# Optimization experiments

Hardware: AMD Instinct MI355X
Metric: run time of the kernel (lower is better)

The kernel has to match this reference:

```python
import jax, jax.numpy as jnp
import numpy as np

N_ACC, N_MER, E = 200000, 100000, 500000
D_ACC, D_MER, H, OUT, CLF = 64, 32, 128, 64, 64
EPS_BN = 1e-5


def _sage(x_src, x_dst, ei, Wl, bl, Wr, n_dst):
    # PyG SAGEConv(aggr='mean', normalize=True): lin_l(mean_agg) + lin_r(x_dst), then L2-normalize rows
    msg = x_src[ei[0]]                                            # [E, d_in] gather
    s = jax.ops.segment_sum(msg, ei[1], num_segments=n_dst)       # [n_dst, d_in]
    cnt = jax.ops.segment_sum(jnp.ones((ei.shape[1],), x_src.dtype), ei[1], num_segments=n_dst)
    mean = s / jnp.maximum(cnt, 1.0)[:, None]
    out = mean @ Wl.T + bl + x_dst @ Wr.T                         # [n_dst, d_out]
    norm = jnp.linalg.norm(out, axis=-1, keepdims=True)
    return out / jnp.maximum(norm, 1e-12)


def _bn(x, g, b):
    # BatchNorm1d in training mode (batch statistics, biased var)
    mu = x.mean(0)
    var = x.var(0)
    return (x - mu) / jnp.sqrt(var + EPS_BN) * g + b


def setup_inputs() -> dict:
    key = jax.random.key(0)
    ks = jax.random.split(key, 40)

    def rn(k, shape, scale=0.05):
        return jax.random.normal(k, shape, dtype=jnp.float32) * scale

    inp = {
        'x_account': jax.random.normal(ks[0], (N_ACC, D_ACC), dtype=jnp.float32),
        'x_merchant': jax.random.normal(ks[1], (N_MER, D_MER), dtype=jnp.float32),
        'ei_pays': jnp.stack([jax.random.randint(ks[2], (E,), 0, N_ACC),
                              jax.random.randint(ks[3], (E,), 0, N_MER)]).astype(jnp.int32),
        'ei_rev': jnp.stack([jax.random.randint(ks[4], (E,), 0, N_MER),
                             jax.random.randint(ks[5], (E,), 0, N_ACC)]).astype(jnp.int32),
        'ei_transfer': jnp.stack([jax.random.randint(ks[6], (E,), 0, N_ACC),
                                  jax.random.randint(ks[7], (E,), 0, N_ACC)]).astype(jnp.int32),
        # input projections (Linear with bias)
        'projW_acc': rn(ks[8], (H, D_ACC)), 'projb_acc': rn(ks[9], (H,)),
        'projW_mer': rn(ks[10], (H, D_MER)), 'projb_mer': rn(ks[11], (H,)),
        # SAGE layer params stacked over 3 edge types [pays, rev_pays, transfers]
        'Wl0': rn(ks[12], (3, H, H)), 'bl0': rn(ks[13], (3, H)), 'Wr0': rn(ks[14], (3, H, H)),
        'Wl1': rn(ks[15], (3, H, H)), 'bl1': rn(ks[16], (3, H)), 'Wr1': rn(ks[17], (3, H, H)),
        'Wl2': rn(ks[18], (3, OUT, H)), 'bl2': rn(ks[19], (3, OUT)), 'Wr2': rn(ks[20], (3, OUT, H)),
        # BN params per layer, stacked over node types [account, merchant]
        'bng0': jnp.ones((2, H), jnp.float32), 'bnb0': jnp.zeros((2, H), jnp.float32),
        'bng1': jnp.ones((2, H), jnp.float32), 'bnb1': jnp.zeros((2, H), jnp.float32),
        'bng2': jnp.ones((2, OUT), jnp.float32), 'bnb2': jnp.zeros((2, OUT), jnp.float32),
        # fraud classifier MLP: Linear(OUT,CLF) -> ReLU -> Linear(CLF,1)
        'clfW1': rn(ks[21], (CLF, OUT)), 'clfb1': rn(ks[22], (CLF,)),
        'clfW2': rn(ks[23], (1, CLF)), 'clfb2': rn(ks[24], (1,)),
    }
    return inp


def reference(x_account, x_merchant, ei_pays, ei_rev, ei_transfer,
              projW_acc, projb_acc, projW_mer, projb_mer,
              Wl0, bl0, Wr0, Wl1, bl1, Wr1, Wl2, bl2, Wr2,
              bng0, bnb0, bng1, bnb1, bng2, bnb2,
              clfW1, clfb1, clfW2, clfb2):
    # input projections
    xa = x_account @ projW_acc.T + projb_acc      # [N_ACC, H]
    xm = x_merchant @ projW_mer.T + projb_mer     # [N_MER, H]

    layers = [(Wl0, bl0, Wr0, bng0, bnb0), (Wl1, bl1, Wr1, bng1, bnb1), (Wl2, bl2, Wr2, bng2, bnb2)]
    n_layers = len(layers)
    for i, (Wl, bl, Wr, g, b) in enumerate(layers):
        # HeteroConv with aggr='sum': sum per-edge-type SAGE outputs per dst node type
        out_mer = _sage(xa, xm, ei_pays, Wl[0], bl[0], Wr[0], N_MER)
        out_acc = (_sage(xm, xa, ei_rev, Wl[1], bl[1], Wr[1], N_ACC)
                   + _sage(xa, xa, ei_transfer, Wl[2], bl[2], Wr[2], N_ACC))
        xa = _bn(out_acc, g[0], b[0])
        xm = _bn(out_mer, g[1], b[1])
        if i < n_layers - 1:
            xa = jax.nn.relu(xa)
            xm = jax.nn.relu(xm)
            # dropout is identity in eval mode

    # classifier head on target node type 'account'
    h = jax.nn.relu(xa @ clfW1.T + clfb1)
    logits = h @ clfW2.T + clfb2                   # [N_ACC, 1]
    return logits
```

## Files before the change

kernel.cpp:

```cpp
#include <hip/hip_runtime.h>
#include <cstdint>
#include <cstddef>

#define EPS_BN 1e-5f
#define CIS_CAP 640

typedef unsigned short ushort_t;
typedef _Float16 h8 __attribute__((ext_vector_type(8)));
typedef __attribute__((ext_vector_type(4))) float f32x4;

static inline int idiv(int a, int b) { return (a + b - 1) / b; }

__device__ __forceinline__ float h2f(ushort_t b) {
  _Float16 h; __builtin_memcpy(&h, &b, 2); return (float)h;
}
__device__ __forceinline__ ushort_t f2h(float x) {
  _Float16 h = (_Float16)x; ushort_t b; __builtin_memcpy(&b, &h, 2); return b;
}
__device__ __forceinline__ float hlo(unsigned u) { return h2f((ushort_t)(u & 0xffffu)); }
__device__ __forceinline__ float hhi(unsigned u) { return h2f((ushort_t)(u >> 16)); }
__device__ __forceinline__ int imin(int a, int b) { return a < b ? a : b; }

__global__ void cnt_kernel(const int* __restrict__ ei, int* __restrict__ cnt, int E) {
  int e = blockIdx.x * 256 + threadIdx.x;
  if (e < E) atomicAdd(&cnt[ei[E + e]], 1);
}

#define SCAN_TPB 256
#define SCAN_EPT 16
#define SCAN_EPB (SCAN_TPB * SCAN_EPT)

__global__ __launch_bounds__(SCAN_TPB) void bsum_kernel(const int* __restrict__ cnt,
                                                        int* __restrict__ bsum, int n) {
  __shared__ int sm[SCAN_TPB];
  int lo = blockIdx.x * SCAN_EPB + threadIdx.x * SCAN_EPT;
  int s = 0;
#pragma unroll
  for (int i = 0; i < SCAN_EPT; ++i) { int idx = lo + i; if (idx < n) s += cnt[idx]; }
  sm[threadIdx.x] = s;
  __syncthreads();
  for (int off = SCAN_TPB / 2; off; off >>= 1) {
    if (threadIdx.x < off) sm[threadIdx.x] += sm[threadIdx.x + off];
    __syncthreads();
  }
  if (threadIdx.x == 0) bsum[blockIdx.x] = sm[0];
}

__global__ __launch_bounds__(1024) void bscan_kernel(int* __restrict__ bsum, int nb) {
  __shared__ int sm[1024];
  int t = threadIdx.x;
  int v = (t < nb) ? bsum[t] : 0;
  sm[t] = v;
  __syncthreads();
  for (int off = 1; off < 1024; off <<= 1) {
    int u = (t >= off) ? sm[t - off] : 0;
    __syncthreads();
    sm[t] += u;
    __syncthreads();
  }
  if (t < nb) bsum[t] = sm[t] - v;
}

__global__ __launch_bounds__(SCAN_TPB) void scatter_scan_kernel(
    int* cntcur, const int* __restrict__ bsum,
    int* __restrict__ row_ptr, int n, int total) {
  __shared__ int sm[SCAN_TPB];
  int t = threadIdx.x;
  int lo = blockIdx.x * SCAN_EPB + t * SCAN_EPT;
  int loc[SCAN_EPT];
  int s = 0;
#pragma unroll
  for (int i = 0; i < SCAN_EPT; ++i) {
    int idx = lo + i;
    int c = (idx < n) ? cntcur[idx] : 0;
    loc[i] = s; s += c;
  }
  sm[t] = s;
  __syncthreads();
  for (int off = 1; off < SCAN_TPB; off <<= 1) {
    int u = (t >= off) ? sm[t - off] : 0;
    __syncthreads();
    sm[t] += u;
    __syncthreads();
  }
  int base = sm[t] - s + bsum[blockIdx.x];
#pragma unroll
  for (int i = 0; i < SCAN_EPT; ++i) {
    int idx = lo + i;
    if (idx < n) { int v = base + loc[i]; row_ptr[idx] = v; cntcur[idx] = v; }
  }
  if (blockIdx.x == 0 && t == 0) row_ptr[n] = total;
}

__global__ void fill_kernel(const int* __restrict__ ei, int* __restrict__ cursor,
                            int* __restrict__ col_idx, int E) {
  int e = blockIdx.x * 256 + threadIdx.x;
  if (e < E) {
    int d = ei[E + e];
    int p = atomicAdd(&cursor[d], 1);
    col_idx[p] = ei[e];
  }
}

__global__ void wprep_kernel(const float* __restrict__ Wl, const float* __restrict__ Wr,
                             ushort_t* __restrict__ dst, int DOUT) {
  int idx = blockIdx.x * 256 + threadIdx.x;
  int per_mat = DOUT * 128;
  int total = 3 * 2 * per_mat;
  if (idx >= total) return;
  int et = idx / (2 * per_mat);
  int r = idx % (2 * per_mat);
  int mat = r / per_mat;
  int e = r % per_mat;
  int nrow = e / 128, k = e % 128;
  const float* src = mat ? Wr : Wl;
  float w = src[et * per_mat + nrow * 128 + k];
  int kt = k >> 5, kk = k & 31;
  int pos = kt * DOUT * 32 + nrow * 32 + kk;
  int MB = 4 * DOUT * 32;
  dst[(size_t)et * (8 * DOUT * 32) + (size_t)mat * MB + pos] = f2h(w);
}

__global__ void wprep_one_kernel(const float* __restrict__ W, ushort_t* __restrict__ dst,
                                 int DOUT, int K) {
  int idx = blockIdx.x * 256 + threadIdx.x;
  if (idx >= DOUT * K) return;
  int row = idx / K, k = idx % K;
  int kt = k >> 5, kk = k & 31;
  dst[kt * DOUT * 32 + row * 32 + kk] = f2h(W[idx]);
}

template<int K>
__global__ __launch_bounds__(256, 4) void proj_mfma_kernel(
    const float* __restrict__ X, const ushort_t* __restrict__ WP,
    const float* __restrict__ bias, ushort_t* __restrict__ out, int n) {
  constexpr int KT = K / 32;
  __shared__ __align__(16) ushort_t ah[32][64];
  const int tid = threadIdx.x, lane = tid & 63, wv = tid >> 6;
  const int base = blockIdx.x * 32;

  if (K == 64) {
    for (int r = wv; r < 32; r += 4) {
      int row = base + r;
      float v = (row < n) ? X[(size_t)row * 64 + lane] : 0.f;
      char* rp = (char*)&ah[r][0];
      int swz = (r & 7) << 4;
      *(ushort_t*)(rp + ((2 * lane) ^ swz)) = f2h(v);
    }
  } else {
    for (int r = wv; r < 16; r += 4) {
      int rr = 2 * r + (lane >> 5);
      int row = base + rr;
      int el = lane & 31;
      float v = (row < n) ? X[(size_t)row * K + el] : 0.f;
      char* rp = (char*)&ah[rr][0];
      int swz = (rr & 7) << 4;
      *(ushort_t*)(rp + ((2 * el) ^ swz)) = f2h(v);
    }
  }
  __syncthreads();

  const int rt = wv >> 1, half = wv & 1;
  const int colbase = half * 64;
  const int cn = lane & 15, g = lane >> 4;

  f32x4 acc[4];
#pragma unroll
  for (int ct = 0; ct < 4; ++ct) {
    float b = bias[colbase + ct * 16 + cn];
    acc[ct] = (f32x4){b, b, b, b};
  }

  const int arow = rt * 16 + cn;
  const char* rowp = (const char*)&ah[arow][0];
  const int swz = (arow & 7) << 4;

#pragma unroll
  for (int kt = 0; kt < KT; ++kt) {
    h8 a = *(const h8*)(rowp + ((kt * 64 + g * 16) ^ swz));
#pragma unroll
    for (int ct = 0; ct < 4; ++ct) {
      int wb = kt * 128 * 32 + (colbase + ct * 16 + cn) * 32 + 8 * g;
      h8 wh = *(const h8*)(WP + wb);
      acc[ct] = __builtin_amdgcn_mfma_f32_16x16x32_f16(a, wh, acc[ct], 0, 0, 0);
    }
  }

#pragma unroll
  for (int i = 0; i < 4; ++i) {
    int rloc = rt * 16 + g * 4 + i;
    int row = base + rloc;
    if (row < n) {
      ushort_t* op = out + (size_t)row * 128 + colbase + cn;
#pragma unroll
      for (int ct = 0; ct < 4; ++ct) op[ct * 16] = f2h(acc[ct][i]);
    }
  }
}

__device__ __forceinline__ void acc8(float* s, uint4 v) {
  s[0] += hlo(v.x); s[1] += hhi(v.x);
  s[2] += hlo(v.y); s[3] += hhi(v.y);
  s[4] += hlo(v.z); s[5] += hhi(v.z);
  s[6] += hlo(v.w); s[7] += hhi(v.w);
}

__device__ __forceinline__ void grp_gather(const int* rps, const int* cis,
                                           const int* __restrict__ gci,
                                           const ushort_t* __restrict__ src,
                                           int rr, int wq, float* s) {
  int b0 = rps[0];
  int p = rps[rr] - b0, e = rps[rr + 1] - b0;
  for (; p + 2 <= e; p += 2) {
    int n0 = (p < CIS_CAP) ? cis[p] : gci[b0 + p];
    int n1 = (p + 1 < CIS_CAP) ? cis[p + 1] : gci[b0 + p + 1];
    uint4 v0 = ((const uint4*)(src + (size_t)n0 * 128))[wq];
    uint4 v1 = ((const uint4*)(src + (size_t)n1 * 128))[wq];
    acc8(s, v0);
    acc8(s, v1);
  }
  if (p < e) {
    int n0 = (p < CIS_CAP) ? cis[p] : gci[b0 + p];
    uint4 v0 = ((const uint4*)(src + (size_t)n0 * 128))[wq];
    acc8(s, v0);
  }
}

__device__ __forceinline__ uint4 pack_h8v(const float* s, float rc) {
  uint4 o;
  o.x = (unsigned)f2h(s[0] * rc) | ((unsigned)f2h(s[1] * rc) << 16);
  o.y = (unsigned)f2h(s[2] * rc) | ((unsigned)f2h(s[3] * rc) << 16);
  o.z = (unsigned)f2h(s[4] * rc) | ((unsigned)f2h(s[5] * rc) << 16);
  o.w = (unsigned)f2h(s[6] * rc) | ((unsigned)f2h(s[7] * rc) << 16);
  return o;
}

template<int DOUT>
__global__ __launch_bounds__(256, 8) void sage_mfma_kernel(
    const int* __restrict__ row_ptr, const int* __restrict__ col_idx,
    const ushort_t* __restrict__ xsrc, const ushort_t* __restrict__ xd,
    const ushort_t* __restrict__ Wb, const float* __restrict__ bl,
    ushort_t* __restrict__ out, int n) {
  constexpr int NCT = DOUT / 32;
  constexpr int MB = 4 * DOUT * 32;
  __shared__ __align__(16) ushort_t am[32][128];
  __shared__ int rps[33];
  __shared__ int cis[CIS_CAP];
  __shared__ float ssb[32][2];
  const int tid = threadIdx.x, lane = tid & 63, wv = tid >> 6;
  const int grp = tid >> 4, wq = tid & 15;
  const int base = blockIdx.x * 32;

  if (tid < 33) rps[tid] = row_ptr[imin(base + tid, n)];
  __syncthreads();
  {
    int b0 = rps[0];
    int lim = imin(rps[32] - b0, CIS_CAP);
    for (int i = tid; i < lim; i += 256) cis[i] = col_idx[b0 + i];
  }
  __syncthreads();

  for (int rr = grp; rr < 32; rr += 16) {
    int row = base + rr;
    float s[8] = {0.f, 0.f, 0.f, 0.f, 0.f, 0.f, 0.f, 0.f};
    if (row < n) grp_gather(rps, cis, col_idx, xsrc, rr, wq, s);
    int deg = rps[rr + 1] - rps[rr];
    float rc = (deg > 0) ? 1.f / (float)deg : 0.f;
    int bo = (wq * 16) ^ ((rr & 7) << 4);
    *(uint4*)((char*)&am[rr][0] + bo) = pack_h8v(s, rc);
  }
  __syncthreads();

  const int rt = wv >> 1, half = wv & 1;
  const int colbase = half * (DOUT / 2);
  const int cn = lane & 15, g = lane >> 4;

  f32x4 acc[NCT];
#pragma unroll
  for (int ct = 0; ct < NCT; ++ct) {
    float b = bl[colbase + ct * 16 + cn];
    acc[ct] = (f32x4){b, b, b, b};
  }

  const int arow = rt * 16 + cn;
  const char* amrow = (const char*)&am[arow][0];
  const int axor = (arow & 7) << 4;
  const ushort_t* xrow = xd + (size_t)imin(base + arow, n - 1) * 128;

#pragma unroll
  for (int kt = 0; kt < 4; ++kt) {
    int aoff = (kt * 64 + g * 16) ^ axor;
    h8 a_m = *(const h8*)(amrow + aoff);
    h8 a_x = *(const h8*)((const char*)xrow + kt * 64 + g * 16);
    int nbase = kt * DOUT * 32 + (colbase + cn) * 32 + 8 * g;
#pragma unroll
    for (int ct = 0; ct < NCT; ++ct) {
      int no = nbase + ct * 16 * 32;
      h8 wl = *(const h8*)(Wb + 0 * MB + no);
      h8 wr = *(const h8*)(Wb + 1 * MB + no);
      acc[ct] = __builtin_amdgcn_mfma_f32_16x16x32_f16(a_m, wl, acc[ct], 0, 0, 0);
      acc[ct] = __builtin_amdgcn_mfma_f32_16x16x32_f16(a_x, wr, acc[ct], 0, 0, 0);
    }
  }

  float p[4];
#pragma unroll
  for (int i = 0; i < 4; ++i) {
    float s = 0.f;
#pragma unroll
    for (int ct = 0; ct < NCT; ++ct) s += acc[ct][i] * acc[ct][i];
#pragma unroll
    for (int m = 1; m < 16; m <<= 1) s += __shfl_xor(s, m);
    p[i] = s;
  }
  if (cn == 0) {
#pragma unroll
    for (int i = 0; i < 4; ++i) ssb[rt * 16 + g * 4 + i][half] = p[i];
  }
  __syncthreads();

#pragma unroll
  for (int i = 0; i < 4; ++i) {
    int rloc = rt * 16 + g * 4 + i;
    int row = base + rloc;
    float ss = ssb[rloc][0] + ssb[rloc][1];
    float rn = 1.0f / fmaxf(sqrtf(ss), 1e-12f);
    if (row < n) {
      ushort_t* op = out + (size_t)row * DOUT + colbase + cn;
#pragma unroll
      for (int ct = 0; ct < NCT; ++ct) op[ct * 16] = f2h(acc[ct][i] * rn);
    }
  }
}

template<int DOUT>
__global__ __launch_bounds__(256, 7) void sage2_mfma_kernel(
    const int* __restrict__ rp1, const int* __restrict__ ci1, const ushort_t* __restrict__ src1,
    const int* __restrict__ rp2, const int* __restrict__ ci2, const ushort_t* __restrict__ src2,
    const ushort_t* __restrict__ Wb1, const ushort_t* __restrict__ Wb2,
    const float* __restrict__ bl1, const float* __restrict__ bl2,
    ushort_t* __restrict__ out, int n) {
  constexpr int NCT = DOUT / 32;
  constexpr int MB = 4 * DOUT * 32;
  __shared__ __align__(16) ushort_t a1[32][128];
  __shared__ __align__(16) ushort_t a2[32][128];
  __shared__ int rps1[33], rps2[33];
  __shared__ int cis1[CIS_CAP], cis2[CIS_CAP];
  __shared__ float ssb1[32][2], ssb2[32][2];
  const int tid = threadIdx.x, lane = tid & 63, wv = tid >> 6;
  const int grp = tid >> 4, wq = tid & 15;
  const int base = blockIdx.x * 32;

  if (tid < 33) rps1[tid] = rp1[imin(base + tid, n)];
  else if (tid < 66) rps2[tid - 33] = rp2[imin(base + (tid - 33), n)];
  __syncthreads();
  {
    int b1 = rps1[0];
    int lim1 = imin(rps1[32] - b1, CIS_CAP);
    for (int i = tid; i < lim1; i += 256) cis1[i] = ci1[b1 + i];
    int b2 = rps2[0];
    int lim2 = imin(rps2[32] - b2, CIS_CAP);
    for (int i = tid; i < lim2; i += 256) cis2[i] = ci2[b2 + i];
  }
  __syncthreads();

  for (int rr = grp; rr < 32; rr += 16) {
    int row = base + rr;
    float s1[8] = {0.f, 0.f, 0.f, 0.f, 0.f, 0.f, 0.f, 0.f};
    float s2[8] = {0.f, 0.f, 0.f, 0.f, 0.f, 0.f, 0.f, 0.f};
    if (row < n) {
      grp_gather(rps1, cis1, ci1, src1, rr, wq, s1);
      grp_gather(rps2, cis2, ci2, src2, rr, wq, s2);
    }
    int d1 = rps1[rr + 1] - rps1[rr];
    int d2 = rps2[rr + 1] - rps2[rr];
    float rc1 = (d1 > 0) ? 1.f / (float)d1 : 0.f;
    float rc2 = (d2 > 0) ? 1.f / (float)d2 : 0.f;
    int bo = (wq * 16) ^ ((rr & 7) << 4);
    *(uint4*)((char*)&a1[rr][0] + bo) = pack_h8v(s1, rc1);
    *(uint4*)((char*)&a2[rr][0] + bo) = pack_h8v(s2, rc2);
  }
  __syncthreads();

  const int rt = wv >> 1, half = wv & 1;
  const int colbase = half * (DOUT / 2);
  const int cn = lane & 15, g = lane >> 4;

  f32x4 acc1[NCT], acc2[NCT];
#pragma unroll
  for (int ct = 0; ct < NCT; ++ct) {
    float b1v = bl1[colbase + ct * 16 + cn];
    float b2v = bl2[colbase + ct * 16 + cn];
    acc1[ct] = (f32x4){b1v, b1v, b1v, b1v};
    acc2[ct] = (f32x4){b2v, b2v, b2v, b2v};
  }

  const int arow = rt * 16 + cn;
  const char* r1 = (const char*)&a1[arow][0];
  const char* r2 = (const char*)&a2[arow][0];
  const int axor = (arow & 7) << 4;
  const ushort_t* xrow = src2 + (size_t)imin(base + arow, n - 1) * 128;

#pragma unroll
  for (int kt = 0; kt < 4; ++kt) {
    int aoff = (kt * 64 + g * 16) ^ axor;
    h8 f1 = *(const h8*)(r1 + aoff);
    h8 f2 = *(const h8*)(r2 + aoff);
    h8 fx = *(const h8*)((const char*)xrow + kt * 64 + g * 16);
    int nbase = kt * DOUT * 32 + (colbase + cn) * 32 + 8 * g;
#pragma unroll
    for (int ct = 0; ct < NCT; ++ct) {
      int no = nbase + ct * 16 * 32;
      h8 wl1 = *(const h8*)(Wb1 + 0 * MB + no);
      h8 wr1 = *(const h8*)(Wb1 + 1 * MB + no);
      h8 wl2 = *(const h8*)(Wb2 + 0 * MB + no);
      h8 wr2 = *(const h8*)(Wb2 + 1 * MB + no);
      acc1[ct] = __builtin_amdgcn_mfma_f32_16x16x32_f16(f1, wl1, acc1[ct], 0, 0, 0);
      acc1[ct] = __builtin_amdgcn_mfma_f32_16x16x32_f16(fx, wr1, acc1[ct], 0, 0, 0);
      acc2[ct] = __builtin_amdgcn_mfma_f32_16x16x32_f16(f2, wl2, acc2[ct], 0, 0, 0);
      acc2[ct] = __builtin_amdgcn_mfma_f32_16x16x32_f16(fx, wr2, acc2[ct], 0, 0, 0);
    }
  }

#pragma unroll
  for (int i = 0; i < 4; ++i) {
    float s1 = 0.f, s2 = 0.f;
#pragma unroll
    for (int ct = 0; ct < NCT; ++ct) {
      s1 += acc1[ct][i] * acc1[ct][i];
      s2 += acc2[ct][i] * acc2[ct][i];
    }
#pragma unroll
    for (int m = 1; m < 16; m <<= 1) {
      s1 += __shfl_xor(s1, m);
      s2 += __shfl_xor(s2, m);
    }
    if (cn == 0) {
      ssb1[rt * 16 + g * 4 + i][half] = s1;
      ssb2[rt * 16 + g * 4 + i][half] = s2;
    }
  }
  __syncthreads();

#pragma unroll
  for (int i = 0; i < 4; ++i) {
    int rloc = rt * 16 + g * 4 + i;
    int row = base + rloc;
    float rn1 = 1.0f / fmaxf(sqrtf(ssb1[rloc][0] + ssb1[rloc][1]), 1e-12f);
    float rn2 = 1.0f / fmaxf(sqrtf(ssb2[rloc][0] + ssb2[rloc][1]), 1e-12f);
    if (row < n) {
      ushort_t* op = out + (size_t)row * DOUT + colbase + cn;
#pragma unroll
      for (int ct = 0; ct < NCT; ++ct)
        op[ct * 16] = f2h(acc1[ct][i] * rn1 + acc2[ct][i] * rn2);
    }
  }
}

template<int C>
__global__ __launch_bounds__(256) void bn_stats_kernel(const ushort_t* __restrict__ x,
    float* __restrict__ stats, int n) {
  constexpr int TPR = C / 8;
  constexpr int RPB = 256 / TPR;
  __shared__ float smw[4][TPR][16];
  const int tid = threadIdx.x, lane = tid & 63, wv = tid >> 6;
  const int cg = tid % TPR;
  const int r0 = tid / TPR;

  float s[8] = {0.f, 0.f, 0.f, 0.f, 0.f, 0.f, 0.f, 0.f};
  float q[8] = {0.f, 0.f, 0.f, 0.f, 0.f, 0.f, 0.f, 0.f};
  for (int r = blockIdx.x * RPB + r0; r < n; r += gridDim.x * RPB) {
    uint4 v = ((const uint4*)(x + (size_t)r * C))[cg];
    unsigned w[4] = {v.x, v.y, v.z, v.w};
#pragma unroll
    for (int j = 0; j < 4; ++j) {
      float a = hlo(w[j]), b = hhi(w[j]);
      s[2 * j] += a; q[2 * j] += a * a;
      s[2 * j + 1] += b; q[2 * j + 1] += b * b;
    }
  }
#pragma unroll
  for (int j = 0; j < 8; ++j) {
    for (int m = TPR; m < 64; m <<= 1) {
      s[j] += __shfl_xor(s[j], m);
      q[j] += __shfl_xor(q[j], m);
    }
  }
  if (lane < TPR) {
#pragma unroll
    for (int j = 0; j < 8; ++j) {
      smw[wv][lane][j] = s[j];
      smw[wv][lane][8 + j] = q[j];
    }
  }
  __syncthreads();
  if (tid < C) {
    int g2 = tid >> 3, j = tid & 7;
    float ts = smw[0][g2][j] + smw[1][g2][j] + smw[2][g2][j] + smw[3][g2][j];
    float tq = smw[0][g2][8 + j] + smw[1][g2][8 + j] + smw[2][g2][8 + j] + smw[3][g2][8 + j];
    atomicAdd(&stats[tid], ts);
    atomicAdd(&stats[C + tid], tq);
  }
}

template<int C, bool RELU>
__global__ __launch_bounds__(256) void bn_apply_kernel(ushort_t* __restrict__ x,
    const float* __restrict__ stats, const float* __restrict__ g,
    const float* __restrict__ b, int n) {
  size_t i = (size_t)blockIdx.x * 256 + threadIdx.x;
  size_t total = (size_t)n * C / 8;
  if (i >= total) return;
  int c0 = (int)((i * 8) & (C - 1));
  float rn = 1.f / (float)n;
  uint4 v = ((const uint4*)x)[i];
  unsigned w[4] = {v.x, v.y, v.z, v.w};
  unsigned o[4];
#pragma unroll
  for (int j = 0; j < 4; ++j) {
    int cA = c0 + 2 * j, cB = cA + 1;
    float muA = stats[cA] * rn, muB = stats[cB] * rn;
    float vaA = stats[C + cA] * rn - muA * muA;
    float vaB = stats[C + cB] * rn - muB * muB;
    float xA = (hlo(w[j]) - muA) * rsqrtf(vaA + EPS_BN) * g[cA] + b[cA];
    float xB = (hhi(w[j]) - muB) * rsqrtf(vaB + EPS_BN) * g[cB] + b[cB];
    if (RELU) { xA = fmaxf(xA, 0.f); xB = fmaxf(xB, 0.f); }
    o[j] = (unsigned)f2h(xA) | ((unsigned)f2h(xB) << 16);
  }
  ((uint4*)x)[i] = make_uint4(o[0], o[1], o[2], o[3]);
}

__global__ __launch_bounds__(256, 4) void clf_mfma_kernel(
    const ushort_t* __restrict__ X, const ushort_t* __restrict__ WPc,
    const float* __restrict__ b1, const float* __restrict__ W2,
    const float* __restrict__ b2, float* __restrict__ out, int n) {
  __shared__ __align__(16) ushort_t axl[32][64];
  __shared__ float ssb[32][2];
  const int tid = threadIdx.x, lane = tid & 63, wv = tid >> 6;
  const int base = blockIdx.x * 32;

  for (int r = wv; r < 16; r += 4) {
    int rr = 2 * r + (lane >> 5);
    int row = base + rr;
    int el = lane & 31;
    unsigned v = (row < n) ? ((const unsigned*)(X + (size_t)row * 64))[el] : 0u;
    int swz = (rr & 7) << 4;
    *(unsigned*)((char*)&axl[rr][0] + ((4 * el) ^ swz)) = v;
  }
  __syncthreads();

  const int rt = wv >> 1, half = wv & 1;
  const int colbase = half * 32;
  const int cn = lane & 15, g = lane >> 4;

  f32x4 acc[2];
#pragma unroll
  for (int ct = 0; ct < 2; ++ct) {
    float b = b1[colbase + ct * 16 + cn];
    acc[ct] = (f32x4){b, b, b, b};
  }

  const int arow = rt * 16 + cn;
  const char* rowp = (const char*)&axl[arow][0];
  const int swz = (arow & 7) << 4;

#pragma unroll
  for (int kt = 0; kt < 2; ++kt) {
    h8 a = *(const h8*)(rowp + ((kt * 64 + g * 16) ^ swz));
#pragma unroll
    for (int ct = 0; ct < 2; ++ct) {
      int wb = kt * 64 * 32 + (colbase + ct * 16 + cn) * 32 + 8 * g;
      h8 wh = *(const h8*)(WPc + wb);
      acc[ct] = __builtin_amdgcn_mfma_f32_16x16x32_f16(a, wh, acc[ct], 0, 0, 0);
    }
  }

  float w2v0 = W2[colbase + cn], w2v1 = W2[colbase + 16 + cn];
#pragma unroll
  for (int i = 0; i < 4; ++i) {
    float p = fmaxf(acc[0][i], 0.f) * w2v0 + fmaxf(acc[1][i], 0.f) * w2v1;
#pragma unroll
    for (int m = 1; m < 16; m <<= 1) p += __shfl_xor(p, m);
    if (cn == 0) ssb[rt * 16 + g * 4 + i][half] = p;
  }
  __syncthreads();

  if (tid < 32) {
    int row = base + tid;
    if (row < n) out[row] = ssb[tid][0] + ssb[tid][1] + b2[0];
  }
}

template<int DO, bool RELU>
static void run_layer(const ushort_t* WB, const float* bl,
                      const float* g, const float* b,
                      const ushort_t* xa, const ushort_t* xm,
                      ushort_t* oa, ushort_t* om, float* STATS,
                      const int* rp_p, const int* ci_p,
                      const int* rp_r, const int* ci_r,
                      const int* rp_t, const int* ci_t,
                      int NA, int NM, hipStream_t stream) {
  const size_t ETS = (size_t)8 * DO * 32;
  float* stA = STATS;
  float* stM = STATS + 2 * DO;
  hipMemsetAsync(STATS, 0, 4 * DO * sizeof(float), stream);
  sage_mfma_kernel<DO><<<idiv(NM, 32), 256, 0, stream>>>(
      rp_p, ci_p, xa, xm, WB + 0 * ETS, bl, om, NM);
  sage2_mfma_kernel<DO><<<idiv(NA, 32), 256, 0, stream>>>(
      rp_r, ci_r, xm, rp_t, ci_t, xa,
      WB + 1 * ETS, WB + 2 * ETS, bl + DO, bl + 2 * DO, oa, NA);
  bn_stats_kernel<DO><<<256, 256, 0, stream>>>(oa, stA, NA);
  bn_stats_kernel<DO><<<256, 256, 0, stream>>>(om, stM, NM);
  bn_apply_kernel<DO, RELU><<<idiv(NA * DO / 8, 256), 256, 0, stream>>>(oa, stA, g, b, NA);
  bn_apply_kernel<DO, RELU><<<idiv(NM * DO / 8, 256), 256, 0, stream>>>(om, stM, g + DO, b + DO, NM);
}

static size_t ws_need(int NA, int NM, int E) {
  size_t acts = ((size_t)2 * NA * 128 + (size_t)2 * NM * 128) * 2;
  size_t wbuf = ((size_t)2 * 98304 + 49152 + 8192 + 4096 + 4096) * 2;
  size_t stats = 1024 * 4;
  size_t ints = ((size_t)(NM + 1) + NM + E
               + 2 * ((size_t)(NA + 1) + NA + E) + 1024) * 4;
  return acts + wbuf + stats + ints + 256;
}

extern "C" void kernel_launch(void* const* d_in, const int* in_sizes, int n_in,
                              void* d_out, int out_size, void* d_ws, size_t ws_size,
                              hipStream_t stream) {
  const int NA = in_sizes[0] / 64;
  const int NM = in_sizes[1] / 32;
  const int E  = in_sizes[2] / 2;
  if (ws_size < ws_need(NA, NM, E)) return;

  const float* x_acc = (const float*)d_in[0];
  const float* x_mer = (const float*)d_in[1];
  const int* ei_pays = (const int*)d_in[2];
  const int* ei_rev  = (const int*)d_in[3];
  const int* ei_tr   = (const int*)d_in[4];
  const float* pWa = (const float*)d_in[5];
  const float* pba = (const float*)d_in[6];
  const float* pWm = (const float*)d_in[7];
  const float* pbm = (const float*)d_in[8];
  const float* Wl[3]  = {(const float*)d_in[9],  (const float*)d_in[12], (const float*)d_in[15]};
  const float* blp[3] = {(const float*)d_in[10], (const float*)d_in[13], (const float*)d_in[16]};
  const float* Wr[3]  = {(const float*)d_in[11], (const float*)d_in[14], (const float*)d_in[17]};
  const float* bng[3] = {(const float*)d_in[18], (const float*)d_in[20], (const float*)d_in[22]};
  const float* bnb[3] = {(const float*)d_in[19], (const float*)d_in[21], (const float*)d_in[23]};
  const float* cW1 = (const float*)d_in[24];
  const float* cb1 = (const float*)d_in[25];
  const float* cW2 = (const float*)d_in[26];
  const float* cb2 = (const float*)d_in[27];

  char* p = (char*)d_ws;
  ushort_t* A0 = (ushort_t*)p; p += (size_t)NA * 128 * 2;
  ushort_t* A1 = (ushort_t*)p; p += (size_t)NA * 128 * 2;
  ushort_t* M0 = (ushort_t*)p; p += (size_t)NM * 128 * 2;
  ushort_t* M1 = (ushort_t*)p; p += (size_t)NM * 128 * 2;
  ushort_t* WB0 = (ushort_t*)p; p += (size_t)98304 * 2;
  ushort_t* WB1 = (ushort_t*)p; p += (size_t)98304 * 2;
  ushort_t* WB2 = (ushort_t*)p; p += (size_t)49152 * 2;
  ushort_t* WPA = (ushort_t*)p; p += (size_t)8192 * 2;
  ushort_t* WPM = (ushort_t*)p; p += (size_t)4096 * 2;
  ushort_t* WPC = (ushort_t*)p; p += (size_t)4096 * 2;
  p = (char*)(((uintptr_t)p + 15) & ~(uintptr_t)15);
  float* STATS = (float*)p; p += 1024 * 4;
  int* rp_p  = (int*)p; p += ((size_t)NM + 1) * 4;
  int* cur_p = (int*)p; p += (size_t)NM * 4;
  int* ci_p  = (int*)p; p += (size_t)E * 4;
  int* rp_r  = (int*)p; p += ((size_t)NA + 1) * 4;
  int* cur_r = (int*)p; p += (size_t)NA * 4;
  int* ci_r  = (int*)p; p += (size_t)E * 4;
  int* rp_t  = (int*)p; p += ((size_t)NA + 1) * 4;
  int* cur_t = (int*)p; p += (size_t)NA * 4;
  int* ci_t  = (int*)p; p += (size_t)E * 4;
  int* bsum  = (int*)p; p += 1024 * 4;

  struct ET { const int* ei; int nd; int* rp; int* cur; int* ci; };
  ET et[3] = {
      {ei_pays, NM, rp_p, cur_p, ci_p},
      {ei_rev,  NA, rp_r, cur_r, ci_r},
      {ei_tr,   NA, rp_t, cur_t, ci_t},
  };
  for (int t = 0; t < 3; ++t) {
    hipMemsetAsync(et[t].cur, 0, (size_t)et[t].nd * sizeof(int), stream);
    cnt_kernel<<<idiv(E, 256), 256, 0, stream>>>(et[t].ei, et[t].cur, E);
    int nb = idiv(et[t].nd, SCAN_EPB);
    bsum_kernel<<<nb, SCAN_TPB, 0, stream>>>(et[t].cur, bsum, et[t].nd);
    bscan_kernel<<<1, 1024, 0, stream>>>(bsum, nb);
    scatter_scan_kernel<<<nb, SCAN_TPB, 0, stream>>>(et[t].cur, bsum, et[t].rp,
                                                     et[t].nd, E);
    fill_kernel<<<idiv(E, 256), 256, 0, stream>>>(et[t].ei, et[t].cur, et[t].ci, E);
  }

  wprep_kernel<<<idiv(3 * 2 * 128 * 128, 256), 256, 0, stream>>>(Wl[0], Wr[0], WB0, 128);
  wprep_kernel<<<idiv(3 * 2 * 128 * 128, 256), 256, 0, stream>>>(Wl[1], Wr[1], WB1, 128);
  wprep_kernel<<<idiv(3 * 2 * 64 * 128, 256), 256, 0, stream>>>(Wl[2], Wr[2], WB2, 64);
  wprep_one_kernel<<<idiv(128 * 64, 256), 256, 0, stream>>>(pWa, WPA, 128, 64);
  wprep_one_kernel<<<idiv(128 * 32, 256), 256, 0, stream>>>(pWm, WPM, 128, 32);
  wprep_one_kernel<<<idiv(64 * 64, 256), 256, 0, stream>>>(cW1, WPC, 64, 64);

  proj_mfma_kernel<64><<<idiv(NA, 32), 256, 0, stream>>>(x_acc, WPA, pba, A0, NA);
  proj_mfma_kernel<32><<<idiv(NM, 32), 256, 0, stream>>>(x_mer, WPM, pbm, M0, NM);

  ushort_t *xa = A0, *xm = M0, *oa = A1, *om = M1;
  run_layer<128, true>(WB0, blp[0], bng[0], bnb[0], xa, xm, oa, om, STATS,
                       rp_p, ci_p, rp_r, ci_r, rp_t, ci_t, NA, NM, stream);
  { ushort_t* t = xa; xa = oa; oa = t; t = xm; xm = om; om = t; }
  run_layer<128, true>(WB1, blp[1], bng[1], bnb[1], xa, xm, oa, om, STATS,
                       rp_p, ci_p, rp_r, ci_r, rp_t, ci_t, NA, NM, stream);
  { ushort_t* t = xa; xa = oa; oa = t; t = xm; xm = om; om = t; }
  run_layer<64, false>(WB2, blp[2], bng[2], bnb[2], xa, xm, oa, om, STATS,
                       rp_p, ci_p, rp_r, ci_r, rp_t, ci_t, NA, NM, stream);
  { ushort_t* t = xa; xa = oa; oa = t; t = xm; xm = om; om = t; }

  clf_mfma_kernel<<<idiv(NA, 32), 256, 0, stream>>>(xa, WPC, cb1, cW2, cb2,
                                                    (float*)d_out, NA);
}
```

Before: 974.7 us.

## Batch per-edge-type CSR build and per-layer kernels into fewer launches

Merges the three per-edge-type CSR construction pipelines (count, block-sum, scan, scatter, fill) into single launches that dispatch on block index. Within each layer, the merchant SAGE kernel and the account dual-SAGE kernel become one grid, and the two BN stats and two BN apply launches are each combined. All per-layer stats buffers are zeroed once up front with one memset, and the cursor arrays are made contiguous so a single memset clears them. This is meant to cut launch count and idle tails between small kernels, at the cost of branchy block dispatch and a lower occupancy bound for the merchant blocks.

```diff
diff --git a/kernel.cpp b/kernel.cpp
--- a/kernel.cpp
+++ b/kernel.cpp
@@ -21,19 +21,33 @@
 __device__ __forceinline__ float hhi(unsigned u) { return h2f((ushort_t)(u >> 16)); }
 __device__ __forceinline__ int imin(int a, int b) { return a < b ? a : b; }
 
-__global__ void cnt_kernel(const int* __restrict__ ei, int* __restrict__ cnt, int E) {
-  int e = blockIdx.x * 256 + threadIdx.x;
-  if (e < E) atomicAdd(&cnt[ei[E + e]], 1);
+__global__ void cnt3_kernel(const int* __restrict__ ei0, int* __restrict__ c0,
+                            const int* __restrict__ ei1, int* __restrict__ c1,
+                            const int* __restrict__ ei2, int* __restrict__ c2,
+                            int E, int nbPer) {
+  int type = blockIdx.x / nbPer;
+  int e = (blockIdx.x % nbPer) * 256 + threadIdx.x;
+  if (e >= E) return;
+  const int* ei = (type == 0) ? ei0 : ((type == 1) ? ei1 : ei2);
+  int* c = (type == 0) ? c0 : ((type == 1) ? c1 : c2);
+  atomicAdd(&c[ei[E + e]], 1);
 }
 
 #define SCAN_TPB 256
 #define SCAN_EPT 16
 #define SCAN_EPB (SCAN_TPB * SCAN_EPT)
 
-__global__ __launch_bounds__(SCAN_TPB) void bsum_kernel(const int* __restrict__ cnt,
-                                                        int* __restrict__ bsum, int n) {
+__global__ __launch_bounds__(SCAN_TPB) void bsum3_kernel(
+    const int* __restrict__ c0, int n0, const int* __restrict__ c1, int n1,
+    const int* __restrict__ c2, int n2, int* __restrict__ bsum,
+    int nb0, int nb1) {
   __shared__ int sm[SCAN_TPB];
-  int lo = blockIdx.x * SCAN_EPB + threadIdx.x * SCAN_EPT;
+  int bid = blockIdx.x;
+  const int* cnt; int n; int* bs; int lb;
+  if (bid < nb0) { cnt = c0; n = n0; bs = bsum; lb = bid; }
+  else if (bid < nb0 + nb1) { cnt = c1; n = n1; bs = bsum + 128; lb = bid - nb0; }
+  else { cnt = c2; n = n2; bs = bsum + 256; lb = bid - nb0 - nb1; }
+  int lo = lb * SCAN_EPB + threadIdx.x * SCAN_EPT;
   int s = 0;
 #pragma unroll
   for (int i = 0; i < SCAN_EPT; ++i) { int idx = lo + i; if (idx < n) s += cnt[idx]; }
@@ -43,30 +57,40 @@
     if (threadIdx.x < off) sm[threadIdx.x] += sm[threadIdx.x + off];
     __syncthreads();
   }
-  if (threadIdx.x == 0) bsum[blockIdx.x] = sm[0];
-}
-
-__global__ __launch_bounds__(1024) void bscan_kernel(int* __restrict__ bsum, int nb) {
-  __shared__ int sm[1024];
+  if (threadIdx.x == 0) bs[lb] = sm[0];
+}
+
+__global__ __launch_bounds__(128) void bscan3_kernel(int* __restrict__ bsum,
+                                                     int nb0, int nb1, int nb2) {
+  __shared__ int sm[128];
+  int* bs = bsum + blockIdx.x * 128;
+  int nb = (blockIdx.x == 0) ? nb0 : ((blockIdx.x == 1) ? nb1 : nb2);
   int t = threadIdx.x;
-  int v = (t < nb) ? bsum[t] : 0;
+  int v = (t < nb) ? bs[t] : 0;
   sm[t] = v;
   __syncthreads();
-  for (int off = 1; off < 1024; off <<= 1) {
+  for (int off = 1; off < 128; off <<= 1) {
     int u = (t >= off) ? sm[t - off] : 0;
     __syncthreads();
     sm[t] += u;
     __syncthreads();
   }
-  if (t < nb) bsum[t] = sm[t] - v;
-}
-
-__global__ __launch_bounds__(SCAN_TPB) void scatter_scan_kernel(
-    int* cntcur, const int* __restrict__ bsum,
-    int* __restrict__ row_ptr, int n, int total) {
+  if (t < nb) bs[t] = sm[t] - v;
+}
+
+__global__ __launch_bounds__(SCAN_TPB) void scatter3_kernel(
+    int* __restrict__ cc0, int* __restrict__ rp0, int n0,
+    int* __restrict__ cc1, int* __restrict__ rp1, int n1,
+    int* __restrict__ cc2, int* __restrict__ rp2, int n2,
+    const int* __restrict__ bsum, int nb0, int nb1, int total) {
   __shared__ int sm[SCAN_TPB];
+  int bid = blockIdx.x;
+  int* cntcur; int* row_ptr; int n; const int* bs; int lb;
+  if (bid < nb0) { cntcur = cc0; row_ptr = rp0; n = n0; bs = bsum; lb = bid; }
+  else if (bid < nb0 + nb1) { cntcur = cc1; row_ptr = rp1; n = n1; bs = bsum + 128; lb = bid - nb0; }
+  else { cntcur = cc2; row_ptr = rp2; n = n2; bs = bsum + 256; lb = bid - nb0 - nb1; }
   int t = threadIdx.x;
-  int lo = blockIdx.x * SCAN_EPB + t * SCAN_EPT;
+  int lo = lb * SCAN_EPB + t * SCAN_EPT;
   int loc[SCAN_EPT];
   int s = 0;
 #pragma unroll
@@ -83,23 +107,28 @@
     sm[t] += u;
     __syncthreads();
   }
-  int base = sm[t] - s + bsum[blockIdx.x];
+  int base = sm[t] - s + bs[lb];
 #pragma unroll
   for (int i = 0; i < SCAN_EPT; ++i) {
     int idx = lo + i;
     if (idx < n) { int v = base + loc[i]; row_ptr[idx] = v; cntcur[idx] = v; }
   }
-  if (blockIdx.x == 0 && t == 0) row_ptr[n] = total;
-}
-
-__global__ void fill_kernel(const int* __restrict__ ei, int* __restrict__ cursor,
-                            int* __restrict__ col_idx, int E) {
-  int e = blockIdx.x * 256 + threadIdx.x;
-  if (e < E) {
-    int d = ei[E + e];
-    int p = atomicAdd(&cursor[d], 1);
-    col_idx[p] = ei[e];
-  }
+  if (lb == 0 && t == 0) row_ptr[n] = total;
+}
+
+__global__ void fill3_kernel(const int* __restrict__ ei0, int* __restrict__ cu0, int* __restrict__ co0,
+                             const int* __restrict__ ei1, int* __restrict__ cu1, int* __restrict__ co1,
+                             const int* __restrict__ ei2, int* __restrict__ cu2, int* __restrict__ co2,
+                             int E, int nbPer) {
+  int type = blockIdx.x / nbPer;
+  int e = (blockIdx.x % nbPer) * 256 + threadIdx.x;
+  if (e >= E) return;
+  const int* ei = (type == 0) ? ei0 : ((type == 1) ? ei1 : ei2);
+  int* cur = (type == 0) ? cu0 : ((type == 1) ? cu1 : cu2);
+  int* ci = (type == 0) ? co0 : ((type == 1) ? co1 : co2);
+  int d = ei[E + e];
+  int p = atomicAdd(&cur[d], 1);
+  ci[p] = ei[e];
 }
 
 __global__ void wprep_kernel(const float* __restrict__ Wl, const float* __restrict__ Wr,
@@ -236,110 +265,17 @@
 }
 
 template<int DOUT>
-__global__ __launch_bounds__(256, 8) void sage_mfma_kernel(
-    const int* __restrict__ row_ptr, const int* __restrict__ col_idx,
-    const ushort_t* __restrict__ xsrc, const ushort_t* __restrict__ xd,
-    const ushort_t* __restrict__ Wb, const float* __restrict__ bl,
-    ushort_t* __restrict__ out, int n) {
-  constexpr int NCT = DOUT / 32;
-  constexpr int MB = 4 * DOUT * 32;
-  __shared__ __align__(16) ushort_t am[32][128];
-  __shared__ int rps[33];
-  __shared__ int cis[CIS_CAP];
-  __shared__ float ssb[32][2];
-  const int tid = threadIdx.x, lane = tid & 63, wv = tid >> 6;
-  const int grp = tid >> 4, wq = tid & 15;
-  const int base = blockIdx.x * 32;
-
-  if (tid < 33) rps[tid] = row_ptr[imin(base + tid, n)];
-  __syncthreads();
-  {
-    int b0 = rps[0];
-    int lim = imin(rps[32] - b0, CIS_CAP);
-    for (int i = tid; i < lim; i += 256) cis[i] = col_idx[b0 + i];
-  }
-  __syncthreads();
-
-  for (int rr = grp; rr < 32; rr += 16) {
-    int row = base + rr;
-    float s[8] = {0.f, 0.f, 0.f, 0.f, 0.f, 0.f, 0.f, 0.f};
-    if (row < n) grp_gather(rps, cis, col_idx, xsrc, rr, wq, s);
-    int deg = rps[rr + 1] - rps[rr];
-    float rc = (deg > 0) ? 1.f / (float)deg : 0.f;
-    int bo = (wq * 16) ^ ((rr & 7) << 4);
-    *(uint4*)((char*)&am[rr][0] + bo) = pack_h8v(s, rc);
-  }
-  __syncthreads();
-
-  const int rt = wv >> 1, half = wv & 1;
-  const int colbase = half * (DOUT / 2);
-  const int cn = lane & 15, g = lane >> 4;
-
-  f32x4 acc[NCT];
-#pragma unroll
-  for (int ct = 0; ct < NCT; ++ct) {
-    float b = bl[colbase + ct * 16 + cn];
-    acc[ct] = (f32x4){b, b, b, b};
-  }
-
-  const int arow = rt * 16 + cn;
-  const char* amrow = (const char*)&am[arow][0];
-  const int axor = (arow & 7) << 4;
-  const ushort_t* xrow = xd + (size_t)imin(base + arow, n - 1) * 128;
-
-#pragma unroll
-  for (int kt = 0; kt < 4; ++kt) {
-    int aoff = (kt * 64 + g * 16) ^ axor;
-    h8 a_m = *(const h8*)(amrow + aoff);
-    h8 a_x = *(const h8*)((const char*)xrow + kt * 64 + g * 16);
-    int nbase = kt * DOUT * 32 + (colbase + cn) * 32 + 8 * g;
-#pragma unroll
-    for (int ct = 0; ct < NCT; ++ct) {
-      int no = nbase + ct * 16 * 32;
-      h8 wl = *(const h8*)(Wb + 0 * MB + no);
-      h8 wr = *(const h8*)(Wb + 1 * MB + no);
-      acc[ct] = __builtin_amdgcn_mfma_f32_16x16x32_f16(a_m, wl, acc[ct], 0, 0, 0);
-      acc[ct] = __builtin_amdgcn_mfma_f32_16x16x32_f16(a_x, wr, acc[ct], 0, 0, 0);
-    }
-  }
-
-  float p[4];
-#pragma unroll
-  for (int i = 0; i < 4; ++i) {
-    float s = 0.f;
-#pragma unroll
-    for (int ct = 0; ct < NCT; ++ct) s += acc[ct][i] * acc[ct][i];
-#pragma unroll
-    for (int m = 1; m < 16; m <<= 1) s += __shfl_xor(s, m);
-    p[i] = s;
-  }
-  if (cn == 0) {
-#pragma unroll
-    for (int i = 0; i < 4; ++i) ssb[rt * 16 + g * 4 + i][half] = p[i];
-  }
-  __syncthreads();
-
-#pragma unroll
-  for (int i = 0; i < 4; ++i) {
-    int rloc = rt * 16 + g * 4 + i;
-    int row = base + rloc;
-    float ss = ssb[rloc][0] + ssb[rloc][1];
-    float rn = 1.0f / fmaxf(sqrtf(ss), 1e-12f);
-    if (row < n) {
-      ushort_t* op = out + (size_t)row * DOUT + colbase + cn;
-#pragma unroll
-      for (int ct = 0; ct < NCT; ++ct) op[ct * 16] = f2h(acc[ct][i] * rn);
-    }
-  }
-}
-
-template<int DOUT>
-__global__ __launch_bounds__(256, 7) void sage2_mfma_kernel(
-    const int* __restrict__ rp1, const int* __restrict__ ci1, const ushort_t* __restrict__ src1,
-    const int* __restrict__ rp2, const int* __restrict__ ci2, const ushort_t* __restrict__ src2,
+__global__ __launch_bounds__(256, 7) void sage_layer_kernel(
+    int nbM,
+    const int* __restrict__ rp_p, const int* __restrict__ ci_p,
+    const ushort_t* __restrict__ xa, const ushort_t* __restrict__ xm,
+    const ushort_t* __restrict__ WbP, const float* __restrict__ blP,
+    ushort_t* __restrict__ om, int NM,
+    const int* __restrict__ rp_r, const int* __restrict__ ci_r,
+    const int* __restrict__ rp_t, const int* __restrict__ ci_t,
     const ushort_t* __restrict__ Wb1, const ushort_t* __restrict__ Wb2,
     const float* __restrict__ bl1, const float* __restrict__ bl2,
-    ushort_t* __restrict__ out, int n) {
+    ushort_t* __restrict__ oa, int NA) {
   constexpr int NCT = DOUT / 32;
   constexpr int MB = 4 * DOUT * 32;
   __shared__ __align__(16) ushort_t a1[32][128];
@@ -349,127 +285,216 @@
   __shared__ float ssb1[32][2], ssb2[32][2];
   const int tid = threadIdx.x, lane = tid & 63, wv = tid >> 6;
   const int grp = tid >> 4, wq = tid & 15;
-  const int base = blockIdx.x * 32;
-
-  if (tid < 33) rps1[tid] = rp1[imin(base + tid, n)];
-  else if (tid < 66) rps2[tid - 33] = rp2[imin(base + (tid - 33), n)];
-  __syncthreads();
-  {
-    int b1 = rps1[0];
-    int lim1 = imin(rps1[32] - b1, CIS_CAP);
-    for (int i = tid; i < lim1; i += 256) cis1[i] = ci1[b1 + i];
-    int b2 = rps2[0];
-    int lim2 = imin(rps2[32] - b2, CIS_CAP);
-    for (int i = tid; i < lim2; i += 256) cis2[i] = ci2[b2 + i];
-  }
-  __syncthreads();
-
-  for (int rr = grp; rr < 32; rr += 16) {
-    int row = base + rr;
-    float s1[8] = {0.f, 0.f, 0.f, 0.f, 0.f, 0.f, 0.f, 0.f};
-    float s2[8] = {0.f, 0.f, 0.f, 0.f, 0.f, 0.f, 0.f, 0.f};
-    if (row < n) {
-      grp_gather(rps1, cis1, ci1, src1, rr, wq, s1);
-      grp_gather(rps2, cis2, ci2, src2, rr, wq, s2);
-    }
-    int d1 = rps1[rr + 1] - rps1[rr];
-    int d2 = rps2[rr + 1] - rps2[rr];
-    float rc1 = (d1 > 0) ? 1.f / (float)d1 : 0.f;
-    float rc2 = (d2 > 0) ? 1.f / (float)d2 : 0.f;
-    int bo = (wq * 16) ^ ((rr & 7) << 4);
-    *(uint4*)((char*)&a1[rr][0] + bo) = pack_h8v(s1, rc1);
-    *(uint4*)((char*)&a2[rr][0] + bo) = pack_h8v(s2, rc2);
-  }
-  __syncthreads();
-
-  const int rt = wv >> 1, half = wv & 1;
-  const int colbase = half * (DOUT / 2);
-  const int cn = lane & 15, g = lane >> 4;
-
-  f32x4 acc1[NCT], acc2[NCT];
-#pragma unroll
-  for (int ct = 0; ct < NCT; ++ct) {
-    float b1v = bl1[colbase + ct * 16 + cn];
-    float b2v = bl2[colbase + ct * 16 + cn];
-    acc1[ct] = (f32x4){b1v, b1v, b1v, b1v};
-    acc2[ct] = (f32x4){b2v, b2v, b2v, b2v};
-  }
-
-  const int arow = rt * 16 + cn;
-  const char* r1 = (const char*)&a1[arow][0];
-  const char* r2 = (const char*)&a2[arow][0];
-  const int axor = (arow & 7) << 4;
-  const ushort_t* xrow = src2 + (size_t)imin(base + arow, n - 1) * 128;
-
-#pragma unroll
-  for (int kt = 0; kt < 4; ++kt) {
-    int aoff = (kt * 64 + g * 16) ^ axor;
-    h8 f1 = *(const h8*)(r1 + aoff);
-    h8 f2 = *(const h8*)(r2 + aoff);
-    h8 fx = *(const h8*)((const char*)xrow + kt * 64 + g * 16);
-    int nbase = kt * DOUT * 32 + (colbase + cn) * 32 + 8 * g;
+
+  if (blockIdx.x < nbM) {
+    const int base = blockIdx.x * 32;
+    if (tid < 33) rps1[tid] = rp_p[imin(base + tid, NM)];
+    __syncthreads();
+    {
+      int b0 = rps1[0];
+      int lim = imin(rps1[32] - b0, CIS_CAP);
+      for (int i = tid; i < lim; i += 256) cis1[i] = ci_p[b0 + i];
+    }
+    __syncthreads();
+
+    for (int rr = grp; rr < 32; rr += 16) {
+      int row = base + rr;
+      float s[8] = {0.f, 0.f, 0.f, 0.f, 0.f, 0.f, 0.f, 0.f};
+      if (row < NM) grp_gather(rps1, cis1, ci_p, xa, rr, wq, s);
+      int deg = rps1[rr + 1] - rps1[rr];
+      float rc = (deg > 0) ? 1.f / (float)deg : 0.f;
+      int bo = (wq * 16) ^ ((rr & 7) << 4);
+      *(uint4*)((char*)&a1[rr][0] + bo) = pack_h8v(s, rc);
+    }
+    __syncthreads();
+
+    const int rt = wv >> 1, half = wv & 1;
+    const int colbase = half * (DOUT / 2);
+    const int cn = lane & 15, g = lane >> 4;
+
+    f32x4 acc[NCT];
 #pragma unroll
     for (int ct = 0; ct < NCT; ++ct) {
-      int no = nbase + ct * 16 * 32;
-      h8 wl1 = *(const h8*)(Wb1 + 0 * MB + no);
-      h8 wr1 = *(const h8*)(Wb1 + 1 * MB + no);
-      h8 wl2 = *(const h8*)(Wb2 + 0 * MB + no);
-      h8 wr2 = *(const h8*)(Wb2 + 1 * MB + no);
-      acc1[ct] = __builtin_amdgcn_mfma_f32_16x16x32_f16(f1, wl1, acc1[ct], 0, 0, 0);
-      acc1[ct] = __builtin_amdgcn_mfma_f32_16x16x32_f16(fx, wr1, acc1[ct], 0, 0, 0);
-      acc2[ct] = __builtin_amdgcn_mfma_f32_16x16x32_f16(f2, wl2, acc2[ct], 0, 0, 0);
-      acc2[ct] = __builtin_amdgcn_mfma_f32_16x16x32_f16(fx, wr2, acc2[ct], 0, 0, 0);
-    }
-  }
-
-#pragma unroll
-  for (int i = 0; i < 4; ++i) {
-    float s1 = 0.f, s2 = 0.f;
+      float b = blP[colbase + ct * 16 + cn];
+      acc[ct] = (f32x4){b, b, b, b};
+    }
+
+    const int arow = rt * 16 + cn;
+    const char* amrow = (const char*)&a1[arow][0];
+    const int axor = (arow & 7) << 4;
+    const ushort_t* xrow = xm + (size_t)imin(base + arow, NM - 1) * 128;
+
+#pragma unroll
+    for (int kt = 0; kt < 4; ++kt) {
+      int aoff = (kt * 64 + g * 16) ^ axor;
+      h8 a_m = *(const h8*)(amrow + aoff);
+      h8 a_x = *(const h8*)((const char*)xrow + kt * 64 + g * 16);
+      int nbase = kt * DOUT * 32 + (colbase + cn) * 32 + 8 * g;
+#pragma unroll
+      for (int ct = 0; ct < NCT; ++ct) {
+        int no = nbase + ct * 16 * 32;
+        h8 wl = *(const h8*)(WbP + 0 * MB + no);
+        h8 wr = *(const h8*)(WbP + 1 * MB + no);
+        acc[ct] = __builtin_amdgcn_mfma_f32_16x16x32_f16(a_m, wl, acc[ct], 0, 0, 0);
+        acc[ct] = __builtin_amdgcn_mfma_f32_16x16x32_f16(a_x, wr, acc[ct], 0, 0, 0);
+      }
+    }
+
+    float p[4];
+#pragma unroll
+    for (int i = 0; i < 4; ++i) {
+      float s = 0.f;
+#pragma unroll
+      for (int ct = 0; ct < NCT; ++ct) s += acc[ct][i] * acc[ct][i];
+#pragma unroll
+      for (int m = 1; m < 16; m <<= 1) s += __shfl_xor(s, m);
+      p[i] = s;
+    }
+    if (cn == 0) {
+#pragma unroll
+      for (int i = 0; i < 4; ++i) ssb1[rt * 16 + g * 4 + i][half] = p[i];
+    }
+    __syncthreads();
+
+#pragma unroll
+    for (int i = 0; i < 4; ++i) {
+      int rloc = rt * 16 + g * 4 + i;
+      int row = base + rloc;
+      float ss = ssb1[rloc][0] + ssb1[rloc][1];
+      float rn = 1.0f / fmaxf(sqrtf(ss), 1e-12f);
+      if (row < NM) {
+        ushort_t* op = om + (size_t)row * DOUT + colbase + cn;
+#pragma unroll
+        for (int ct = 0; ct < NCT; ++ct) op[ct * 16] = f2h(acc[ct][i] * rn);
+      }
+    }
+  } else {
+    const int base = (blockIdx.x - nbM) * 32;
+    if (tid < 33) rps1[tid] = rp_r[imin(base + tid, NA)];
+    else if (tid < 66) rps2[tid - 33] = rp_t[imin(base + (tid - 33), NA)];
+    __syncthreads();
+    {
+      int b1v = rps1[0];
+      int lim1 = imin(rps1[32] - b1v, CIS_CAP);
+      for (int i = tid; i < lim1; i += 256) cis1[i] = ci_r[b1v + i];
+      int b2v = rps2[0];
+      int lim2 = imin(rps2[32] - b2v, CIS_CAP);
+      for (int i = tid; i < lim2; i += 256) cis2[i] = ci_t[b2v + i];
+    }
+    __syncthreads();
+
+    for (int rr = grp; rr < 32; rr += 16) {
+      int row = base + rr;
+      float s1[8] = {0.f, 0.f, 0.f, 0.f, 0.f, 0.f, 0.f, 0.f};
+      float s2[8] = {0.f, 0.f, 0.f, 0.f, 0.f, 0.f, 0.f, 0.f};
+      if (row < NA) {
+        grp_gather(rps1, cis1, ci_r, xm, rr, wq, s1);
+        grp_gather(rps2, cis2, ci_t, xa, rr, wq, s2);
+      }
+      int d1 = rps1[rr + 1] - rps1[rr];
+      int d2 = rps2[rr + 1] - rps2[rr];
+      float rc1 = (d1 > 0) ? 1.f / (float)d1 : 0.f;
+      float rc2 = (d2 > 0) ? 1.f / (float)d2 : 0.f;
+      int bo = (wq * 16) ^ ((rr & 7) << 4);
+      *(uint4*)((char*)&a1[rr][0] + bo) = pack_h8v(s1, rc1);
+      *(uint4*)((char*)&a2[rr][0] + bo) = pack_h8v(s2, rc2);
+    }
+    __syncthreads();
+
+    const int rt = wv >> 1, half = wv & 1;
+    const int colbase = half * (DOUT / 2);
+    const int cn = lane & 15, g = lane >> 4;
+
+    f32x4 acc1[NCT], acc2[NCT];
 #pragma unroll
     for (int ct = 0; ct < NCT; ++ct) {
-      s1 += acc1[ct][i] * acc1[ct][i];
-      s2 += acc2[ct][i] * acc2[ct][i];
-    }
-#pragma unroll
-    for (int m = 1; m < 16; m <<= 1) {
-      s1 += __shfl_xor(s1, m);
-      s2 += __shfl_xor(s2, m);
-    }
-    if (cn == 0) {
-      ssb1[rt * 16 + g * 4 + i][half] = s1;
-      ssb2[rt * 16 + g * 4 + i][half] = s2;
-    }
-  }
-  __syncthreads();
-
-#pragma unroll
-  for (int i = 0; i < 4; ++i) {
-    int rloc = rt * 16 + g * 4 + i;
-    int row = base + rloc;
-    float rn1 = 1.0f / fmaxf(sqrtf(ssb1[rloc][0] + ssb1[rloc][1]), 1e-12f);
-    float rn2 = 1.0f / fmaxf(sqrtf(ssb2[rloc][0] + ssb2[rloc][1]), 1e-12f);
-    if (row < n) {
-      ushort_t* op = out + (size_t)row * DOUT + colbase + cn;
-#pragma unroll
-      for (int ct = 0; ct < NCT; ++ct)
-        op[ct * 16] = f2h(acc1[ct][i] * rn1 + acc2[ct][i] * rn2);
+      float b1b = bl1[colbase + ct * 16 + cn];
+      float b2b = bl2[colbase + ct * 16 + cn];
+      acc1[ct] = (f32x4){b1b, b1b, b1b, b1b};
+      acc2[ct] = (f32x4){b2b, b2b, b2b, b2b};
+    }
+
+    const int arow = rt * 16 + cn;
+    const char* r1p = (const char*)&a1[arow][0];
+    const char* r2p = (const char*)&a2[arow][0];
+    const int axor = (arow & 7) << 4;
+    const ushort_t* xrow = xa + (size_t)imin(base + arow, NA - 1) * 128;
+
+#pragma unroll
+    for (int kt = 0; kt < 4; ++kt) {
+      int aoff = (kt * 64 + g * 16) ^ axor;
+      h8 f1 = *(const h8*)(r1p + aoff);
+      h8 f2 = *(const h8*)(r2p + aoff);
+      h8 fx = *(const h8*)((const char*)xrow + kt * 64 + g * 16);
+      int nbase = kt * DOUT * 32 + (colbase + cn) * 32 + 8 * g;
+#pragma unroll
+      for (int ct = 0; ct < NCT; ++ct) {
+        int no = nbase + ct * 16 * 32;
+        h8 wl1 = *(const h8*)(Wb1 + 0 * MB + no);
+        h8 wr1 = *(const h8*)(Wb1 + 1 * MB + no);
+        h8 wl2 = *(const h8*)(Wb2 + 0 * MB + no);
+        h8 wr2 = *(const h8*)(Wb2 + 1 * MB + no);
+        acc1[ct] = __builtin_amdgcn_mfma_f32_16x16x32_f16(f1, wl1, acc1[ct], 0, 0, 0);
+        acc1[ct] = __builtin_amdgcn_mfma_f32_16x16x32_f16(fx, wr1, acc1[ct], 0, 0, 0);
+        acc2[ct] = __builtin_amdgcn_mfma_f32_16x16x32_f16(f2, wl2, acc2[ct], 0, 0, 0);
+        acc2[ct] = __builtin_amdgcn_mfma_f32_16x16x32_f16(fx, wr2, acc2[ct], 0, 0, 0);
+      }
+    }
+
+#pragma unroll
+    for (int i = 0; i < 4; ++i) {
+      float s1 = 0.f, s2 = 0.f;
+#pragma unroll
+      for (int ct = 0; ct < NCT; ++ct) {
+        s1 += acc1[ct][i] * acc1[ct][i];
+        s2 += acc2[ct][i] * acc2[ct][i];
+      }
+#pragma unroll
+      for (int m = 1; m < 16; m <<= 1) {
+        s1 += __shfl_xor(s1, m);
+        s2 += __shfl_xor(s2, m);
+      }
+      if (cn == 0) {
+        ssb1[rt * 16 + g * 4 + i][half] = s1;
+        ssb2[rt * 16 + g * 4 + i][half] = s2;
+      }
+    }
+    __syncthreads();
+
+#pragma unroll
+    for (int i = 0; i < 4; ++i) {
+      int rloc = rt * 16 + g * 4 + i;
+      int row = base + rloc;
+      float rn1 = 1.0f / fmaxf(sqrtf(ssb1[rloc][0] + ssb1[rloc][1]), 1e-12f);
+      float rn2 = 1.0f / fmaxf(sqrtf(ssb2[rloc][0] + ssb2[rloc][1]), 1e-12f);
+      if (row < NA) {
+        ushort_t* op = oa + (size_t)row * DOUT + colbase + cn;
+#pragma unroll
+        for (int ct = 0; ct < NCT; ++ct)
+          op[ct * 16] = f2h(acc1[ct][i] * rn1 + acc2[ct][i] * rn2);
+      }
     }
   }
 }
 
 template<int C>
-__global__ __launch_bounds__(256) void bn_stats_kernel(const ushort_t* __restrict__ x,
-    float* __restrict__ stats, int n) {
+__global__ __launch_bounds__(256) void bn_stats2_kernel(
+    const ushort_t* __restrict__ xA, float* __restrict__ stA, int nA,
+    const ushort_t* __restrict__ xM, float* __restrict__ stM, int nM) {
   constexpr int TPR = C / 8;
   constexpr int RPB = 256 / TPR;
   __shared__ float smw[4][TPR][16];
+  int bid = blockIdx.x;
+  const ushort_t* x; float* st; int n;
+  if (bid < 256) { x = xA; st = stA; n = nA; }
+  else { bid -= 256; x = xM; st = stM; n = nM; }
   const int tid = threadIdx.x, lane = tid & 63, wv = tid >> 6;
   const int cg = tid % TPR;
   const int r0 = tid / TPR;
 
   float s[8] = {0.f, 0.f, 0.f, 0.f, 0.f, 0.f, 0.f, 0.f};
   float q[8] = {0.f, 0.f, 0.f, 0.f, 0.f, 0.f, 0.f, 0.f};
-  for (int r = blockIdx.x * RPB + r0; r < n; r += gridDim.x * RPB) {
+  for (int r = bid * RPB + r0; r < n; r += 256 * RPB) {
     uint4 v = ((const uint4*)(x + (size_t)r * C))[cg];
     unsigned w[4] = {v.x, v.y, v.z, v.w};
 #pragma unroll
@@ -498,18 +523,27 @@
     int g2 = tid >> 3, j = tid & 7;
     float ts = smw[0][g2][j] + smw[1][g2][j] + smw[2][g2][j] + smw[3][g2][j];
     float tq = smw[0][g2][8 + j] + smw[1][g2][8 + j] + smw[2][g2][8 + j] + smw[3][g2][8 + j];
-    atomicAdd(&stats[tid], ts);
-    atomicAdd(&stats[C + tid], tq);
+    atomicAdd(&st[tid], ts);
+    atomicAdd(&st[C + tid], tq);
   }
 }
 
 template<int C, bool RELU>
-__global__ __launch_bounds__(256) void bn_apply_kernel(ushort_t* __restrict__ x,
-    const float* __restrict__ stats, const float* __restrict__ g,
-    const float* __restrict__ b, int n) {
+__global__ __launch_bounds__(256) void bn_apply2_kernel(
+    ushort_t* __restrict__ xA, const float* __restrict__ stA,
+    const float* __restrict__ gA, const float* __restrict__ bA, int nA,
+    ushort_t* __restrict__ xM, const float* __restrict__ stM,
+    const float* __restrict__ gM, const float* __restrict__ bM, int nM) {
   size_t i = (size_t)blockIdx.x * 256 + threadIdx.x;
-  size_t total = (size_t)n * C / 8;
-  if (i >= total) return;
+  size_t totA = (size_t)nA * C / 8;
+  ushort_t* x; const float *st, *g, *b; int n;
+  if (i < totA) { x = xA; st = stA; g = gA; b = bA; n = nA; }
+  else {
+    i -= totA;
+    size_t totM = (size_t)nM * C / 8;
+    if (i >= totM) return;
+    x = xM; st = stM; g = gM; b = bM; n = nM;
+  }
   int c0 = (int)((i * 8) & (C - 1));
   float rn = 1.f / (float)n;
   uint4 v = ((const uint4*)x)[i];
@@ -518,13 +552,13 @@
 #pragma unroll
   for (int j = 0; j < 4; ++j) {
     int cA = c0 + 2 * j, cB = cA + 1;
-    float muA = stats[cA] * rn, muB = stats[cB] * rn;
-    float vaA = stats[C + cA] * rn - muA * muA;
-    float vaB = stats[C + cB] * rn - muB * muB;
-    float xA = (hlo(w[j]) - muA) * rsqrtf(vaA + EPS_BN) * g[cA] + b[cA];
-    float xB = (hhi(w[j]) - muB) * rsqrtf(vaB + EPS_BN) * g[cB] + b[cB];
-    if (RELU) { xA = fmaxf(xA, 0.f); xB = fmaxf(xB, 0.f); }
-    o[j] = (unsigned)f2h(xA) | ((unsigned)f2h(xB) << 16);
+    float muA = st[cA] * rn, muB = st[cB] * rn;
+    float vaA = st[C + cA] * rn - muA * muA;
+    float vaB = st[C + cB] * rn - muB * muB;
+    float xAv = (hlo(w[j]) - muA) * rsqrtf(vaA + EPS_BN) * g[cA] + b[cA];
+    float xBv = (hhi(w[j]) - muB) * rsqrtf(vaB + EPS_BN) * g[cB] + b[cB];
+    if (RELU) { xAv = fmaxf(xAv, 0.f); xBv = fmaxf(xBv, 0.f); }
+    o[j] = (unsigned)f2h(xAv) | ((unsigned)f2h(xBv) << 16);
   }
   ((uint4*)x)[i] = make_uint4(o[0], o[1], o[2], o[3]);
 }
@@ -602,22 +636,20 @@
   const size_t ETS = (size_t)8 * DO * 32;
   float* stA = STATS;
   float* stM = STATS + 2 * DO;
-  hipMemsetAsync(STATS, 0, 4 * DO * sizeof(float), stream);
-  sage_mfma_kernel<DO><<<idiv(NM, 32), 256, 0, stream>>>(
-      rp_p, ci_p, xa, xm, WB + 0 * ETS, bl, om, NM);
-  sage2_mfma_kernel<DO><<<idiv(NA, 32), 256, 0, stream>>>(
-      rp_r, ci_r, xm, rp_t, ci_t, xa,
-      WB + 1 * ETS, WB + 2 * ETS, bl + DO, bl + 2 * DO, oa, NA);
-  bn_stats_kernel<DO><<<256, 256, 0, stream>>>(oa, stA, NA);
-  bn_stats_kernel<DO><<<256, 256, 0, stream>>>(om, stM, NM);
-  bn_apply_kernel<DO, RELU><<<idiv(NA * DO / 8, 256), 256, 0, stream>>>(oa, stA, g, b, NA);
-  bn_apply_kernel<DO, RELU><<<idiv(NM * DO / 8, 256), 256, 0, stream>>>(om, stM, g + DO, b + DO, NM);
+  int nbM = idiv(NM, 32), nbA = idiv(NA, 32);
+  sage_layer_kernel<DO><<<nbM + nbA, 256, 0, stream>>>(
+      nbM, rp_p, ci_p, xa, xm, WB + 0 * ETS, bl, om, NM,
+      rp_r, ci_r, rp_t, ci_t, WB + 1 * ETS, WB + 2 * ETS,
+      bl + DO, bl + 2 * DO, oa, NA);
+  bn_stats2_kernel<DO><<<512, 256, 0, stream>>>(oa, stA, NA, om, stM, NM);
+  bn_apply2_kernel<DO, RELU><<<idiv((NA + NM) * DO / 8, 256), 256, 0, stream>>>(
+      oa, stA, g, b, NA, om, stM, g + DO, b + DO, NM);
 }
 
 static size_t ws_need(int NA, int NM, int E) {
   size_t acts = ((size_t)2 * NA * 128 + (size_t)2 * NM * 128) * 2;
   size_t wbuf = ((size_t)2 * 98304 + 49152 + 8192 + 4096 + 4096) * 2;
-  size_t stats = 1024 * 4;
+  size_t stats = 3 * 1024 * 4;
   size_t ints = ((size_t)(NM + 1) + NM + E
                + 2 * ((size_t)(NA + 1) + NA + E) + 1024) * 4;
   return acts + wbuf + stats + ints + 256;
@@ -662,34 +694,32 @@
   ushort_t* WPM = (ushort_t*)p; p += (size_t)4096 * 2;
   ushort_t* WPC = (ushort_t*)p; p += (size_t)4096 * 2;
   p = (char*)(((uintptr_t)p + 15) & ~(uintptr_t)15);
-  float* STATS = (float*)p; p += 1024 * 4;
+  float* STATS = (float*)p; p += 3 * 1024 * 4;
+  int* cur_p = (int*)p; p += (size_t)NM * 4;
+  int* cur_r = (int*)p; p += (size_t)NA * 4;
+  int* cur_t = (int*)p; p += (size_t)NA * 4;
   int* rp_p  = (int*)p; p += ((size_t)NM + 1) * 4;
-  int* cur_p = (int*)p; p += (size_t)NM * 4;
   int* ci_p  = (int*)p; p += (size_t)E * 4;
   int* rp_r  = (int*)p; p += ((size_t)NA + 1) * 4;
-  int* cur_r = (int*)p; p += (size_t)NA * 4;
   int* ci_r  = (int*)p; p += (size_t)E * 4;
   int* rp_t  = (int*)p; p += ((size_t)NA + 1) * 4;
-  int* cur_t = (int*)p; p += (size_t)NA * 4;
   int* ci_t  = (int*)p; p += (size_t)E * 4;
   int* bsum  = (int*)p; p += 1024 * 4;
 
-  struct ET { const int* ei; int nd; int* rp; int* cur; int* ci; };
-  ET et[3] = {
-      {ei_pays, NM, rp_p, cur_p, ci_p},
-      {ei_rev,  NA, rp_r, cur_r, ci_r},
-      {ei_tr,   NA, rp_t, cur_t, ci_t},
-  };
-  for (int t = 0; t < 3; ++t) {
-    hipMemsetAsync(et[t].cur, 0, (size_t)et[t].nd * sizeof(int), stream);
-    cnt_kernel<<<idiv(E, 256), 256, 0, stream>>>(et[t].ei, et[t].cur, E);
-    int nb = idiv(et[t].nd, SCAN_EPB);
-    bsum_kernel<<<nb, SCAN_TPB, 0, stream>>>(et[t].cur, bsum, et[t].nd);
-    bscan_kernel<<<1, 1024, 0, stream>>>(bsum, nb);
-    scatter_scan_kernel<<<nb, SCAN_TPB, 0, stream>>>(et[t].cur, bsum, et[t].rp,
-                                                     et[t].nd, E);
-    fill_kernel<<<idiv(E, 256), 256, 0, stream>>>(et[t].ei, et[t].cur, et[t].ci, E);
-  }
+  hipMemsetAsync(cur_p, 0, ((size_t)NM + 2 * (size_t)NA) * sizeof(int), stream);
+  hipMemsetAsync(STATS, 0, 3 * 1024 * sizeof(float), stream);
+  int nbPer = idiv(E, 256);
+  cnt3_kernel<<<3 * nbPer, 256, 0, stream>>>(ei_pays, cur_p, ei_rev, cur_r,
+                                             ei_tr, cur_t, E, nbPer);
+  int nb0 = idiv(NM, SCAN_EPB), nb1 = idiv(NA, SCAN_EPB), nb2 = idiv(NA, SCAN_EPB);
+  bsum3_kernel<<<nb0 + nb1 + nb2, SCAN_TPB, 0, stream>>>(
+      cur_p, NM, cur_r, NA, cur_t, NA, bsum, nb0, nb1);
+  bscan3_kernel<<<3, 128, 0, stream>>>(bsum, nb0, nb1, nb2);
+  scatter3_kernel<<<nb0 + nb1 + nb2, SCAN_TPB, 0, stream>>>(
+      cur_p, rp_p, NM, cur_r, rp_r, NA, cur_t, rp_t, NA, bsum, nb0, nb1, E);
+  fill3_kernel<<<3 * nbPer, 256, 0, stream>>>(ei_pays, cur_p, ci_p,
+                                              ei_rev, cur_r, ci_r,
+                                              ei_tr, cur_t, ci_t, E, nbPer);
 
   wprep_kernel<<<idiv(3 * 2 * 128 * 128, 256), 256, 0, stream>>>(Wl[0], Wr[0], WB0, 128);
   wprep_kernel<<<idiv(3 * 2 * 128 * 128, 256), 256, 0, stream>>>(Wl[1], Wr[1], WB1, 128);
@@ -705,10 +735,10 @@
   run_layer<128, true>(WB0, blp[0], bng[0], bnb[0], xa, xm, oa, om, STATS,
                        rp_p, ci_p, rp_r, ci_r, rp_t, ci_t, NA, NM, stream);
   { ushort_t* t = xa; xa = oa; oa = t; t = xm; xm = om; om = t; }
-  run_layer<128, true>(WB1, blp[1], bng[1], bnb[1], xa, xm, oa, om, STATS,
+  run_layer<128, true>(WB1, blp[1], bng[1], bnb[1], xa, xm, oa, om, STATS + 1024,
                        rp_p, ci_p, rp_r, ci_r, rp_t, ci_t, NA, NM, stream);
   { ushort_t* t = xa; xa = oa; oa = t; t = xm; xm = om; om = t; }
-  run_layer<64, false>(WB2, blp[2], bng[2], bnb[2], xa, xm, oa, om, STATS,
+  run_layer<64, false>(WB2, blp[2], bng[2], bnb[2], xa, xm, oa, om, STATS + 2048,
                        rp_p, ci_p, rp_r, ci_r, rp_t, ci_t, NA, NM, stream);
   { ushort_t* t = xa; xa = oa; oa = t; t = xm; xm = om; om = t; }
 
```

New measurement: 875.5 us. 1.11x faster.
